# Kernel tuning notes

Hardware: AMD Instinct MI355X
Metric: run time of the kernel (lower is better)

Reference implementation:

```python
import jax, jax.numpy as jnp
import numpy as np
import math

D_MODEL = 1024
H = 16
D_K = D_MODEL // H
D_FF = 4096
NEG = -1e9


def layer_norm(x, alpha, bias):
    # Faithful to source: mean over last dim, UNBIASED std (torch.std default),
    # eps defined in source but never used in forward.
    mean = jnp.mean(x, axis=-1, keepdims=True)
    std = jnp.std(x, axis=-1, ddof=1, keepdims=True)
    return (x - mean) / std * alpha + bias


def mha(x, mask, w_q, w_k, w_v, w_o):
    B, S, D = x.shape
    q = (x @ w_q.T).reshape(B, S, H, D_K)
    k = (x @ w_k.T).reshape(B, S, H, D_K)
    v = (x @ w_v.T).reshape(B, S, H, D_K)
    scores = jnp.einsum('bqhd,bkhd->bhqk', q, k) / math.sqrt(D_K)
    scores = jnp.where(mask, NEG, scores)
    attn = jax.nn.softmax(scores, axis=-1)
    out = jnp.einsum('bhqk,bkhd->bqhd', attn, v).reshape(B, S, D)
    return out @ w_o.T


def setup_inputs() -> dict:
    key = jax.random.key(0)
    ks = jax.random.split(key, 16)
    B, S = 4, 2048
    s = 0.02
    return {
        'x': jax.random.normal(ks[0], (B, S, D_MODEL), jnp.float32),
        'w_q': jax.random.normal(ks[1], (D_MODEL, D_MODEL), jnp.float32) * s,
        'w_k': jax.random.normal(ks[2], (D_MODEL, D_MODEL), jnp.float32) * s,
        'w_v': jax.random.normal(ks[3], (D_MODEL, D_MODEL), jnp.float32) * s,
        'w_o': jax.random.normal(ks[4], (D_MODEL, D_MODEL), jnp.float32) * s,
        'l1_w': jax.random.normal(ks[5], (D_FF, D_MODEL), jnp.float32) * s,
        'l1_b': jnp.zeros((D_FF,), jnp.float32),
        'l2_w': jax.random.normal(ks[6], (D_MODEL, D_FF), jnp.float32) * s,
        'l2_b': jnp.zeros((D_MODEL,), jnp.float32),
        'norm1_a': jnp.ones((D_MODEL,), jnp.float32),
        'norm1_b': jnp.zeros((D_MODEL,), jnp.float32),
        'norm2_a': jnp.ones((D_MODEL,), jnp.float32),
        'norm2_b': jnp.zeros((D_MODEL,), jnp.float32),
        'normf_a': jnp.ones((D_MODEL,), jnp.float32),
        'normf_b': jnp.zeros((D_MODEL,), jnp.float32),
        'mask': jax.random.randint(ks[7], (B, 1, 1, S), 0, 2) == 1,
    }


def reference(x, w_q, w_k, w_v, w_o, l1_w, l1_b, l2_w, l2_b,
              norm1_a, norm1_b, norm2_a, norm2_b, normf_a, normf_b, mask):
    # residual 1: pre-norm self-attention (dropout is identity at eval)
    x = x + mha(layer_norm(x, norm1_a, norm1_b), mask, w_q, w_k, w_v, w_o)
    # residual 2: pre-norm FFN
    h = layer_norm(x, norm2_a, norm2_b)
    ff = jax.nn.relu(h @ l1_w.T + l1_b) @ l2_w.T + l2_b
    x = x + ff
    return layer_norm(x, normf_a, normf_b)
```

## Files before the change

kernel.cpp:

```cpp
#include <hip/hip_runtime.h>
#include <hip/hip_bf16.h>


typedef __bf16 bf16x8 __attribute__((ext_vector_type(8)));
typedef float f32x4 __attribute__((ext_vector_type(4)));
typedef unsigned short u16x8 __attribute__((ext_vector_type(8)));
using bf16 = __hip_bfloat16;

__device__ __forceinline__ f32x4 mfma16(bf16x8 a, bf16x8 b, f32x4 c) {
  return __builtin_amdgcn_mfma_f32_16x16x32_bf16(a, b, c, 0, 0, 0);
}

__device__ __forceinline__ int swz(int row, int blk) {
  return row * 64 + ((blk ^ (row & 7)) << 3);
}

__device__ __forceinline__ void stage_tile64(unsigned short* lds,
                                             const bf16* g, int ld, int rows) {
  const int lane = threadIdx.x & 63, wid = threadIdx.x >> 6;
  const int r8 = lane >> 3, blk = lane & 7;
  const bf16* gl = g + (size_t)r8 * ld + ((blk ^ r8) << 3);
  const int passes = rows >> 3;
  for (int p = wid; p < passes; p += 4) {
    __builtin_amdgcn_global_load_lds(
        (const __attribute__((address_space(1))) void*)(gl + (size_t)(p * 8) * ld),
        (__attribute__((address_space(3))) void*)(lds + p * 512),
        16, 0, 0);
  }
}

__device__ __forceinline__ void stage_half512(unsigned short* lds,
                                              const bf16* g, int ld) {
  const int lane = threadIdx.x & 63, w8 = threadIdx.x >> 6;
  const int r8 = lane >> 3, blk = lane & 7;
  const bf16* gl = g + (size_t)r8 * ld + ((blk ^ r8) << 3);
  __builtin_amdgcn_global_load_lds(
      (const __attribute__((address_space(1))) void*)(gl + (size_t)(w8 * 8) * ld),
      (__attribute__((address_space(3))) void*)(lds + w8 * 512), 16, 0, 0);
  __builtin_amdgcn_global_load_lds(
      (const __attribute__((address_space(1))) void*)(gl + (size_t)((w8 + 8) * 8) * ld),
      (__attribute__((address_space(3))) void*)(lds + (w8 + 8) * 512), 16, 0, 0);
}

__device__ __forceinline__ short bfb(float x) {
  return (short)__hip_bfloat16_raw(__float2bfloat16(x)).x;
}

__global__ __launch_bounds__(256) void cvt_all_k(
    const float* __restrict__ wq, const float* __restrict__ wk,
    const float* __restrict__ wv, const float* __restrict__ wo,
    const float* __restrict__ l1, const float* __restrict__ l2,
    bf16* __restrict__ WQKV, bf16* __restrict__ WO, bf16* __restrict__ L1W,
    bf16* __restrict__ L2W) {
  const int bid = blockIdx.x;
  const float* s;
  bf16* d;
  int lb;
  if (bid < 1024) {
    s = wq; d = WQKV; lb = bid;
  } else if (bid < 2048) {
    s = wk; d = WQKV + (1 << 20); lb = bid - 1024;
  } else if (bid < 3072) {
    s = wv; d = WQKV + (2 << 20); lb = bid - 2048;
  } else if (bid < 4096) {
    s = wo; d = WO; lb = bid - 3072;
  } else if (bid < 8192) {
    s = l1; d = L1W; lb = bid - 4096;
  } else {
    s = l2; d = L2W; lb = bid - 8192;
  }
  const int i = lb * 1024 + threadIdx.x * 4;
  const float4 v = *reinterpret_cast<const float4*>(s + i);
  ushort4 o;
  o.x = (unsigned short)bfb(v.x);
  o.y = (unsigned short)bfb(v.y);
  o.z = (unsigned short)bfb(v.z);
  o.w = (unsigned short)bfb(v.w);
  *reinterpret_cast<ushort4*>(d + i) = o;
}

template <bool OUT_F32>
__global__ __launch_bounds__(256) void layernorm_k(const float* __restrict__ in,
                                                   const float* __restrict__ gamma,
                                                   const float* __restrict__ beta,
                                                   void* __restrict__ out) {
  __shared__ float red[8];
  const int row = blockIdx.x, t = threadIdx.x;
  const float4 vv = reinterpret_cast<const float4*>(in + (size_t)row * 1024)[t];
  const float x0 = vv.x, x1 = vv.y, x2 = vv.z, x3 = vv.w;
  float s = x0 + x1 + x2 + x3;
#pragma unroll
  for (int off = 32; off; off >>= 1) s += __shfl_down(s, off);
  if ((t & 63) == 0) red[t >> 6] = s;
  __syncthreads();
  const float mean = (red[0] + red[1] + red[2] + red[3]) * (1.0f / 1024.0f);
  const float d0 = x0 - mean, d1 = x1 - mean, d2 = x2 - mean, d3 = x3 - mean;
  float sq = d0 * d0 + d1 * d1 + d2 * d2 + d3 * d3;
#pragma unroll
  for (int off = 32; off; off >>= 1) sq += __shfl_down(sq, off);
  if ((t & 63) == 0) red[4 + (t >> 6)] = sq;
  __syncthreads();
  const float var =
      fmaxf((red[4] + red[5] + red[6] + red[7]) * (1.0f / 1023.0f), 1e-20f);
  const float rstd = rsqrtf(var);
  const float4 ga = reinterpret_cast<const float4*>(gamma)[t];
  const float4 be = reinterpret_cast<const float4*>(beta)[t];
  const float y0 = d0 * rstd * ga.x + be.x;
  const float y1 = d1 * rstd * ga.y + be.y;
  const float y2 = d2 * rstd * ga.z + be.z;
  const float y3 = d3 * rstd * ga.w + be.w;
  if (OUT_F32) {
    reinterpret_cast<float4*>((float*)out + (size_t)row * 1024)[t] =
        make_float4(y0, y1, y2, y3);
  } else {
    ushort4 o;
    o.x = (unsigned short)bfb(y0);
    o.y = (unsigned short)bfb(y1);
    o.z = (unsigned short)bfb(y2);
    o.w = (unsigned short)bfb(y3);
    reinterpret_cast<ushort4*>((bf16*)out + (size_t)row * 1024)[t] = o;
  }
}

template <bool HAS_BIAS, bool RELU, bool HAS_RES, bool OUT_F32>
__global__ __launch_bounds__(256) void gemm_bt(const bf16* __restrict__ A,
                                               const bf16* __restrict__ W,
                                               const float* __restrict__ bias,
                                               const float* __restrict__ resid,
                                               void* __restrict__ out,
                                               int M, int N, int K,
                                               int lda, int ldw) {
  __shared__ __align__(16) unsigned short As[128 * 64];
  __shared__ __align__(16) unsigned short Bs[128 * 64];
  const int lane = threadIdx.x & 63, wid = threadIdx.x >> 6;
  const int n16 = lane & 15, quad = lane >> 4;
  const int wm = (wid >> 1) * 64, wn = (wid & 1) * 64;
  const int tm = blockIdx.x * 128, tn = blockIdx.y * 128;
  f32x4 acc[4][4] = {};
  for (int k0 = 0; k0 < K; k0 += 64) {
    stage_tile64(As, A + (size_t)tm * lda + k0, lda, 128);
    stage_tile64(Bs, W + (size_t)tn * ldw + k0, ldw, 128);
    __syncthreads();
#pragma unroll
    for (int kk = 0; kk < 64; kk += 32) {
      bf16x8 af[4], bw[4];
#pragma unroll
      for (int i = 0; i < 4; ++i)
        af[i] = *reinterpret_cast<const bf16x8*>(
            &As[swz(wm + i * 16 + n16, (kk >> 3) + quad)]);
#pragma unroll
      for (int j = 0; j < 4; ++j)
        bw[j] = *reinterpret_cast<const bf16x8*>(
            &Bs[swz(wn + j * 16 + n16, (kk >> 3) + quad)]);
#pragma unroll
      for (int i = 0; i < 4; ++i)
#pragma unroll
        for (int j = 0; j < 4; ++j) acc[i][j] = mfma16(af[i], bw[j], acc[i][j]);
    }
    __syncthreads();
  }
#pragma unroll
  for (int i = 0; i < 4; ++i) {
#pragma unroll
    for (int j = 0; j < 4; ++j) {
      const int n = tn + wn + j * 16 + n16;
      const float bv = HAS_BIAS ? bias[n] : 0.0f;
#pragma unroll
      for (int r = 0; r < 4; ++r) {
        const int m = tm + wm + i * 16 + quad * 4 + r;
        float vv = acc[i][j][r] + bv;
        if (RELU) vv = fmaxf(vv, 0.0f);
        if (HAS_RES) vv += resid[(size_t)m * N + n];
        if (OUT_F32)
          ((float*)out)[(size_t)m * N + n] = vv;
        else
          ((bf16*)out)[(size_t)m * N + n] = __float2bfloat16(vv);
      }
    }
  }
}

#define PHASE3(LAB, LBB, QB, DO_B, STAGES, WAITS)                              \
  {                                                                            \
    const unsigned short* LA = (LAB) + lasel * 8192;                           \
    if (DO_B) {                                                                \
      const unsigned short* LB = (LBB) + lbsel * 8192;                         \
      _Pragma("unroll") for (int j = 0; j < 4; ++j) {                          \
        const int br = bloc + j * 16 + n16;                                    \
        bfr[j][0] = *reinterpret_cast<const bf16x8*>(&LB[swz(br, quad)]);      \
        bfr[j][1] = *reinterpret_cast<const bf16x8*>(&LB[swz(br, 4 + quad)]);  \
      }                                                                        \
    }                                                                          \
    bf16x8 a0[4], a1[4];                                                       \
    _Pragma("unroll") for (int ii = 0; ii < 4; ++ii) {                         \
      const int ar = ((QB)*2 + ii) * 16 + n16;                                 \
      a0[ii] = *reinterpret_cast<const bf16x8*>(&LA[swz(ar, quad)]);           \
      a1[ii] = *reinterpret_cast<const bf16x8*>(&LA[swz(ar, 4 + quad)]);       \
    }                                                                          \
    STAGES;                                                                    \
    WAITS;                                                                     \
    __builtin_amdgcn_sched_barrier(0);                                         \
    __builtin_amdgcn_s_barrier();                                              \
    asm volatile("s_waitcnt lgkmcnt(0)" ::: "memory");                         \
    __builtin_amdgcn_sched_barrier(0);                                         \
    __builtin_amdgcn_s_setprio(1);                                             \
    _Pragma("unroll") for (int ii = 0; ii < 4; ++ii)                           \
        _Pragma("unroll") for (int j = 0; j < 4; ++j) {                        \
      f32x4 c = acc[(QB)*2 + ii][j];                                           \
      c = mfma16(a0[ii], bfr[j][0], c);                                        \
      c = mfma16(a1[ii], bfr[j][1], c);                                        \
      acc[(QB)*2 + ii][j] = c;                                                 \
    }                                                                          \
    __builtin_amdgcn_s_setprio(0);                                             \
    __builtin_amdgcn_sched_barrier(0);                                         \
    __builtin_amdgcn_s_barrier();                                              \
  }

template <bool QKV, bool HAS_BIAS, bool RELU>
__global__ __launch_bounds__(512, 1) void gemm256_k(
    const bf16* __restrict__ A0p, const bf16* __restrict__ cln,
    const bf16* __restrict__ W, const float* __restrict__ bias,
    const int* __restrict__ cnt, bf16* __restrict__ out,
    bf16* __restrict__ kvout, int M, int N, int K, int lda, int ldw) {
  __shared__ __align__(16) unsigned short Lds[81920];
  const int tm = blockIdx.x * 256;
  const int tn = blockIdx.y * 256;
  const bf16* A = A0p;
  bool isQ = true;
  if (QKV) {
    isQ = (blockIdx.y < 4);
    if (!isQ) {
      const int npad = (cnt[tm >> 11] + 127) & ~127;
      if ((tm & 2047) >= npad) return;
      A = cln;
    }
  }
  const int lane = threadIdx.x & 63, w8 = threadIdx.x >> 6;
  const int n16 = lane & 15, quad = lane >> 4;
  const int wm = (w8 >> 2) << 7;
  const int wn = (w8 & 3) << 6;
  const int lasel = wm >> 7, lbsel = wn >> 7, bloc = wn & 127;
  const int NTT = K >> 6;
  const bf16* Ag = A + (size_t)tm * lda;
  const bf16* Wg = W + (size_t)tn * ldw;
  f32x4 acc[8][4] = {};

  auto STAGEA = [&](int slot, int tile) {
    unsigned short* dst = Lds + slot * 16384;
    stage_half512(dst, Ag + tile * 64, lda);
    stage_half512(dst + 8192, Ag + (size_t)128 * lda + tile * 64, lda);
  };
  auto STAGEB = [&](int slot, int tile) {
    unsigned short* dst = Lds + 49152 + slot * 16384;
    stage_half512(dst, Wg + tile * 64, ldw);
    stage_half512(dst + 8192, Wg + (size_t)128 * ldw + tile * 64, ldw);
  };

  STAGEA(0, 0); STAGEB(0, 0);
  STAGEA(1, 1); STAGEB(1, 1);
  asm volatile("s_waitcnt vmcnt(8)" ::: "memory");
  __builtin_amdgcn_sched_barrier(0);
  __builtin_amdgcn_s_barrier();

  int sA = 0;
  for (int i = 0; i < NTT; i += 2) {
    const bool hasNext = (i + 2 < NTT);
    const int sA1 = (sA + 1 == 3) ? 0 : sA + 1;
    const int sA2 = (sA1 + 1 == 3) ? 0 : sA1 + 1;
    const unsigned short* LAi = Lds + sA * 16384;
    const unsigned short* LAi1 = Lds + sA1 * 16384;
    const unsigned short* LB0 = Lds + 49152;
    const unsigned short* LB1 = Lds + 49152 + 16384;
    bf16x8 bfr[4][2];
    PHASE3(LAi, LB0, 0, true, if (hasNext) STAGEA(sA2, i + 2), );
    PHASE3(LAi, LB0, 2, false, if (hasNext) STAGEB(0, i + 2),
           if (hasNext) { asm volatile("s_waitcnt vmcnt(8)" ::: "memory"); }
           else { asm volatile("s_waitcnt vmcnt(0)" ::: "memory"); });
    PHASE3(LAi1, LB1, 0, true, if (hasNext) STAGEA(sA, i + 3), );
    PHASE3(LAi1, LB1, 2, false, if (hasNext) STAGEB(1, i + 3),
           if (hasNext) { asm volatile("s_waitcnt vmcnt(8)" ::: "memory"); });
    sA = sA2;
  }
  bf16* op;
  int ldo, nc0;
  if (QKV && !isQ) {
    op = kvout; ldo = 2048; nc0 = tn - 1024;
  } else if (QKV) {
    op = out; ldo = 1024; nc0 = tn;
  } else {
    op = out; ldo = N; nc0 = tn;
  }
#pragma unroll
  for (int i = 0; i < 8; ++i) {
#pragma unroll
    for (int j = 0; j < 4; ++j) {
      const int n = nc0 + wn + j * 16 + n16;
      const float bv = HAS_BIAS ? bias[n] : 0.0f;
#pragma unroll
      for (int r = 0; r < 4; ++r) {
        const int m = tm + wm + i * 16 + quad * 4 + r;
        float vv = acc[i][j][r] + bv;
        if (RELU) vv = fmaxf(vv, 0.0f);
        op[(size_t)m * ldo + n] = __float2bfloat16(vv);
      }
    }
  }
}

__global__ __launch_bounds__(256) void prep_mask_k(const int* __restrict__ m,
                                                   float* __restrict__ mf,
                                                   int n) {
  __shared__ int s;
  if (threadIdx.x == 0) s = 0;
  __syncthreads();
  unsigned int acc = 0;
  for (int i = threadIdx.x; i < 512; i += 256)
    acc |= ((const unsigned int*)m)[i] & 0xFFFFFF00u;
  if (acc) atomicOr(&s, 1);
  __syncthreads();
  const bool bytes = (s != 0);
  const int i = blockIdx.x * 256 + threadIdx.x;
  if (i < n) {
    const int v = bytes ? (int)((const unsigned char*)m)[i] : m[i];
    mf[i] = v ? -1.4427e9f : 0.0f;
  }
}

__global__ __launch_bounds__(256) void scan_k(const float* __restrict__ maskf,
                                              float* __restrict__ cmask,
                                              int* __restrict__ idx,
                                              int* __restrict__ cnt) {
  __shared__ int wsum[4];
  const int b = blockIdx.x, t = threadIdx.x, lane = t & 63, w = t >> 6;
  const float* mrow = maskf + b * 2048;
  int keep[8], local = 0;
#pragma unroll
  for (int e = 0; e < 8; ++e) {
    keep[e] = (mrow[t * 8 + e] == 0.0f) ? 1 : 0;
    local += keep[e];
  }
  int inc = local;
#pragma unroll
  for (int off = 1; off < 64; off <<= 1) {
    int v = __shfl_up(inc, off);
    if (lane >= off) inc += v;
  }
  if (lane == 63) wsum[w] = inc;
  __syncthreads();
  int base = 0;
#pragma unroll
  for (int i = 0; i < 4; ++i)
    if (i < w) base += wsum[i];
  int p = base + inc - local;
#pragma unroll
  for (int e = 0; e < 8; ++e)
    if (keep[e]) idx[b * 2048 + p++] = t * 8 + e;
  const int total = wsum[0] + wsum[1] + wsum[2] + wsum[3];
  if (t == 0) cnt[b] = total;
  for (int i = t; i < 2048; i += 256)
    cmask[b * 2048 + i] = (i < total) ? 0.0f : -1.4427e9f;
}

__global__ __launch_bounds__(128) void gatherA_k(const bf16* __restrict__ ln1,
                                                 const int* __restrict__ idx,
                                                 const int* __restrict__ cnt,
                                                 bf16* __restrict__ cln) {
  const int b = blockIdx.x >> 11, j = blockIdx.x & 2047;
  const int n = cnt[b];
  const int npad = (n + 127) & ~127;
  if (j >= npad) return;
  u16x8* dst = reinterpret_cast<u16x8*>(cln + ((size_t)(b * 2048 + j)) * 1024);
  if (j < n) {
    const int s = idx[b * 2048 + j];
    const u16x8* src =
        reinterpret_cast<const u16x8*>(ln1 + ((size_t)(b * 2048 + s)) * 1024);
    dst[threadIdx.x] = src[threadIdx.x];
  } else {
    u16x8 z = {};
    dst[threadIdx.x] = z;
  }
}

__global__ __launch_bounds__(256) void attn_k(const bf16* __restrict__ q,
                                              const bf16* __restrict__ kv,
                                              const float* __restrict__ cmask,
                                              const int* __restrict__ cnt,
                                              bf16* __restrict__ out, int BHN) {
  __shared__ __align__(16) unsigned short Ks[2][64 * 64];
  __shared__ __align__(16) unsigned short Vs[2][64 * 72];
  const int lane = threadIdx.x & 63, wid = threadIdx.x >> 6;
  const int n16 = lane & 15, quad = lane >> 4;
  const int bid0 = blockIdx.x;
  const int nwg = gridDim.x;
  const int bid = (bid0 & 7) * (nwg >> 3) + (bid0 >> 3);
  const int qb = bid & 15, bh = bid >> 4;
  const int b = bh >> 4, h = bh & 15;
  const bf16* qp0 = q + (size_t)b * 2048 * 1024 + h * 64;
  const bf16* kp0 = kv + (size_t)b * 2048 * 2048 + h * 64;
  const bf16* vp0 = kp0 + 1024;
  const float* mfb = cmask + b * 2048;
  const int cntb = cnt[b];
  const int nk = ((cntb + 63) >> 6) << 6;
  const int qrow0 = qb * 128 + wid * 32;

  bf16x8 qf[2][2];
#pragma unroll
  for (int g = 0; g < 2; ++g) {
    const bf16* qp = qp0 + (size_t)(qrow0 + g * 16 + n16) * 1024 + quad * 8;
    qf[g][0] = *reinterpret_cast<const bf16x8*>(qp);
    qf[g][1] = *reinterpret_cast<const bf16x8*>(qp + 32);
  }
  bf16x8 ones;
#pragma unroll
  for (int e = 0; e < 8; ++e) ones[e] = (__bf16)1.0f;
  f32x4 oacc[2][4] = {};
  f32x4 lacc[2] = {};
  const int prow = ((n16 >> 2) << 3) + (n16 & 3);
  const int vkey = lane, vdc = wid * 16;

  stage_tile64(Ks[0], kp0, 2048, 64);
  {
    const bf16* vp = vp0 + (size_t)vkey * 2048 + vdc;
    const u16x8 a = *reinterpret_cast<const u16x8*>(vp);
    const u16x8 bq = *reinterpret_cast<const u16x8*>(vp + 8);
#pragma unroll
    for (int e = 0; e < 8; ++e) {
      Vs[0][(vdc + e) * 72 + vkey] = a[e];
      Vs[0][(vdc + 8 + e) * 72 + vkey] = bq[e];
    }
  }
  int cur = 0;
  for (int kt = 0; kt < nk; kt += 64) {
    __syncthreads();
    const bool hasNext = (kt + 64 < nk);
    const bool fullTile = (kt + 64 <= cntb);
    u16x8 na = {}, nb = {};
    if (hasNext) {
      stage_tile64(Ks[cur ^ 1], kp0 + (size_t)(kt + 64) * 2048, 2048, 64);
      const bf16* vp = vp0 + (size_t)(kt + 64 + vkey) * 2048 + vdc;
      na = *reinterpret_cast<const u16x8*>(vp);
      nb = *reinterpret_cast<const u16x8*>(vp + 8);
    }
    const unsigned short* Kc = Ks[cur];
    const unsigned short* Vc = Vs[cur];
#pragma unroll
    for (int sub = 0; sub < 2; ++sub) {
      const int kb = sub * 32;
      bf16x8 aflo[2], afhi[2];
#pragma unroll
      for (int st = 0; st < 2; ++st) {
        const int row = kb + prow + st * 4;
        aflo[st] = *reinterpret_cast<const bf16x8*>(&Kc[swz(row, quad)]);
        afhi[st] = *reinterpret_cast<const bf16x8*>(&Kc[swz(row, 4 + quad)]);
      }
      __builtin_amdgcn_s_setprio(1);
      f32x4 z[2][2];
#pragma unroll
      for (int g = 0; g < 2; ++g)
#pragma unroll
        for (int st = 0; st < 2; ++st) {
          f32x4 zz = {};
          zz = mfma16(aflo[st], qf[g][0], zz);
          zz = mfma16(afhi[st], qf[g][1], zz);
          z[g][st] = zz;
        }
      __builtin_amdgcn_s_setprio(0);
      float4 m0 = make_float4(0.f, 0.f, 0.f, 0.f);
      float4 m1 = make_float4(0.f, 0.f, 0.f, 0.f);
      if (!fullTile) {
        m0 = *reinterpret_cast<const float4*>(mfb + kt + kb + quad * 8);
        m1 = *reinterpret_cast<const float4*>(mfb + kt + kb + quad * 8 + 4);
      }
      bf16x8 vf[4];
#pragma unroll
      for (int j = 0; j < 4; ++j)
        vf[j] = *reinterpret_cast<const bf16x8*>(
            &Vc[(j * 16 + n16) * 72 + kb + quad * 8]);
#pragma unroll
      for (int g = 0; g < 2; ++g) {
        bf16x8 pf;
#pragma unroll
        for (int r = 0; r < 4; ++r) {
          const float e0 = __builtin_amdgcn_exp2f(
              fmaf(z[g][0][r], 0.18033688f, ((const float*)&m0)[r]));
          const float e1 = __builtin_amdgcn_exp2f(
              fmaf(z[g][1][r], 0.18033688f, ((const float*)&m1)[r]));
          pf[r] = (__bf16)e0;
          pf[4 + r] = (__bf16)e1;
        }
        __builtin_amdgcn_s_setprio(1);
#pragma unroll
        for (int j = 0; j < 4; ++j) oacc[g][j] = mfma16(pf, vf[j], oacc[g][j]);
        lacc[g] = mfma16(pf, ones, lacc[g]);
        __builtin_amdgcn_s_setprio(0);
      }
    }
    if (hasNext) {
      unsigned short* Vn = Vs[cur ^ 1];
#pragma unroll
      for (int e = 0; e < 8; ++e) {
        Vn[(vdc + e) * 72 + vkey] = na[e];
        Vn[(vdc + 8 + e) * 72 + vkey] = nb[e];
      }
    }
    cur ^= 1;
  }
#pragma unroll
  for (int g = 0; g < 2; ++g) {
#pragma unroll
    for (int r = 0; r < 4; ++r) {
      const float lr = 1.0f / fmaxf(lacc[g][r], 1e-20f);
      bf16* op =
          out + (size_t)(b * 2048 + qrow0 + g * 16 + quad * 4 + r) * 1024 +
          h * 64;
#pragma unroll
      for (int j = 0; j < 4; ++j)
        op[j * 16 + n16] = __float2bfloat16(oacc[g][j][r] * lr);
    }
  }
}

extern "C" void kernel_launch(void* const* d_in, const int* in_sizes, int n_in,
                              void* d_out, int out_size, void* d_ws,
                              size_t ws_size, hipStream_t stream) {
  const float* x    = (const float*)d_in[0];
  const float* w_q  = (const float*)d_in[1];
  const float* w_k  = (const float*)d_in[2];
  const float* w_v  = (const float*)d_in[3];
  const float* w_o  = (const float*)d_in[4];
  const float* l1_w = (const float*)d_in[5];
  const float* l1_b = (const float*)d_in[6];
  const float* l2_w = (const float*)d_in[7];
  const float* l2_b = (const float*)d_in[8];
  const float* n1a  = (const float*)d_in[9];
  const float* n1b  = (const float*)d_in[10];
  const float* n2a  = (const float*)d_in[11];
  const float* n2b  = (const float*)d_in[12];
  const float* nfa  = (const float*)d_in[13];
  const float* nfb  = (const float*)d_in[14];
  const int* mask   = (const int*)d_in[15];

  const int D = 1024, FF = 4096;
  const int M = in_sizes[0] / D;
  const int B = M / 2048;

  const size_t MB = 1024ull * 1024ull;
  if (ws_size < 121 * MB) return;
  char* w = (char*)d_ws;
  bf16* WQKV = (bf16*)(w + 0 * MB);
  bf16* WO   = (bf16*)(w + 6 * MB);
  bf16* L1W  = (bf16*)(w + 8 * MB);
  bf16* L2W  = (bf16*)(w + 16 * MB);
  bf16* LN1  = (bf16*)(w + 24 * MB);
  bf16* Qbuf = (bf16*)(w + 40 * MB);
  bf16* ATT  = LN1;
  bf16* HLN  = (bf16*)(w + 40 * MB);
  bf16* CLN  = (bf16*)(w + 56 * MB);
  bf16* FF1  = (bf16*)(w + 56 * MB);
  bf16* KV   = (bf16*)(w + 88 * MB);
  float* X1  = (float*)(w + 88 * MB);
  float* MASKF = (float*)(w + 120 * MB);
  float* CMASK = (float*)(w + 120 * MB + 256 * 1024);
  int*   IDX   = (int*)(w + 120 * MB + 512 * 1024);
  int*   CNT   = (int*)(w + 120 * MB + 768 * 1024);

  const dim3 blk(256);
  cvt_all_k<<<dim3(12288), blk, 0, stream>>>(w_q, w_k, w_v, w_o, l1_w, l2_w,
                                             WQKV, WO, L1W, L2W);
  prep_mask_k<<<dim3((M + 255) / 256), blk, 0, stream>>>(mask, MASKF, M);
  scan_k<<<dim3(B), blk, 0, stream>>>(MASKF, CMASK, IDX, CNT);

  layernorm_k<false><<<M, blk, 0, stream>>>(x, n1a, n1b, LN1);
  gatherA_k<<<dim3(B * 2048), dim3(128), 0, stream>>>(LN1, IDX, CNT, CLN);
  gemm256_k<true, false, false><<<dim3(M / 256, 12), dim3(512), 0, stream>>>(
      LN1, CLN, WQKV, nullptr, CNT, Qbuf, KV, M, 3072, 1024, 1024, 1024);
  const int BHN = B * 16;
  attn_k<<<dim3((M / 128) * 16), blk, 0, stream>>>(Qbuf, KV, CMASK, CNT, ATT,
                                                   BHN);
  gemm_bt<false, false, true, true><<<dim3(M / 128, D / 128), blk, 0, stream>>>(
      ATT, WO, nullptr, x, X1, M, D, D, D, D);
  layernorm_k<false><<<M, blk, 0, stream>>>(X1, n2a, n2b, HLN);
  for (int c = 0; c < 2; ++c) {
    gemm256_k<false, true, true><<<dim3(M / 256, 8), dim3(512), 0, stream>>>(
        HLN, nullptr, L1W + (size_t)c * 2048 * D, l1_b + c * 2048, nullptr,
        FF1, nullptr, M, 2048, 1024, 1024, 1024);
    if (c == 0)
      gemm_bt<true, false, true, true>
          <<<dim3(M / 128, D / 128), blk, 0, stream>>>(
              FF1, L2W + c * 2048, l2_b, X1, X1, M, D, 2048, 2048, FF);
    else
      gemm_bt<false, false, true, true>
          <<<dim3(M / 128, D / 128), blk, 0, stream>>>(
              FF1, L2W + c * 2048, nullptr, X1, X1, M, D, 2048, 2048, FF);
  }
  layernorm_k<true><<<M, blk, 0, stream>>>(X1, nfa, nfb, (float*)d_out);
}
```

Measured before the change: 493.4 us.

## Fuse mask prep into scan, scatter LN1 rows directly, and unsplit FFN GEMMs

Mask prep and the prefix scan now run as one kernel that emits per-row ranks and zero-pads the compacted buffer. The first layernorm scatters kept rows into it, which removes the separate gather kernel. The FFN runs as a single full-width up-projection whose output is spread across eight 512-column chunks in free workspace, followed by one down-projection GEMM. The earlier two-chunk loop with its extra residual read-modify-write pass is gone, and the l2 weight conversion moves later so its buffer can reuse space. It also folds the softmax scale into the Q projection and skips mask loads on full attention tiles. The cost is a more intricate workspace aliasing scheme and indirect chunked A addressing.

```diff
diff --git a/kernel.cpp b/kernel.cpp
--- a/kernel.cpp
+++ b/kernel.cpp
@@ -6,6 +6,8 @@
 typedef float f32x4 __attribute__((ext_vector_type(4)));
 typedef unsigned short u16x8 __attribute__((ext_vector_type(8)));
 using bf16 = __hip_bfloat16;
+
+struct Tab8 { bf16* p[8]; };
 
 __device__ __forceinline__ f32x4 mfma16(bf16x8 a, bf16x8 b, f32x4 c) {
   return __builtin_amdgcn_mfma_f32_16x16x32_bf16(a, b, c, 0, 0, 0);
@@ -46,12 +48,25 @@
   return (short)__hip_bfloat16_raw(__float2bfloat16(x)).x;
 }
 
-__global__ __launch_bounds__(256) void cvt_all_k(
+__global__ __launch_bounds__(256) void cvt_k(const float* __restrict__ s,
+                                             bf16* __restrict__ d, int n) {
+  const int i = (blockIdx.x * 256 + threadIdx.x) * 4;
+  if (i + 3 < n) {
+    const float4 v = *reinterpret_cast<const float4*>(s + i);
+    ushort4 o;
+    o.x = (unsigned short)bfb(v.x);
+    o.y = (unsigned short)bfb(v.y);
+    o.z = (unsigned short)bfb(v.z);
+    o.w = (unsigned short)bfb(v.w);
+    *reinterpret_cast<ushort4*>(d + i) = o;
+  }
+}
+
+__global__ __launch_bounds__(256) void cvt_main_k(
     const float* __restrict__ wq, const float* __restrict__ wk,
     const float* __restrict__ wv, const float* __restrict__ wo,
-    const float* __restrict__ l1, const float* __restrict__ l2,
-    bf16* __restrict__ WQKV, bf16* __restrict__ WO, bf16* __restrict__ L1W,
-    bf16* __restrict__ L2W) {
+    const float* __restrict__ l1, bf16* __restrict__ WQKV,
+    bf16* __restrict__ WO, bf16* __restrict__ L1W) {
   const int bid = blockIdx.x;
   const float* s;
   bf16* d;
@@ -64,10 +79,8 @@
     s = wv; d = WQKV + (2 << 20); lb = bid - 2048;
   } else if (bid < 4096) {
     s = wo; d = WO; lb = bid - 3072;
-  } else if (bid < 8192) {
+  } else {
     s = l1; d = L1W; lb = bid - 4096;
-  } else {
-    s = l2; d = L2W; lb = bid - 8192;
   }
   const int i = lb * 1024 + threadIdx.x * 4;
   const float4 v = *reinterpret_cast<const float4*>(s + i);
@@ -79,11 +92,69 @@
   *reinterpret_cast<ushort4*>(d + i) = o;
 }
 
-template <bool OUT_F32>
+__global__ __launch_bounds__(256) void scan2_k(const int* __restrict__ m,
+                                               float* __restrict__ cmask,
+                                               int* __restrict__ rank,
+                                               int* __restrict__ cnt,
+                                               bf16* __restrict__ cln) {
+  __shared__ int wsum[4];
+  __shared__ int sflag;
+  const int b = blockIdx.x, t = threadIdx.x, lane = t & 63, w = t >> 6;
+  if (t == 0) sflag = 0;
+  __syncthreads();
+  unsigned int acc = 0;
+  for (int i = t; i < 512; i += 256)
+    acc |= ((const unsigned int*)m)[i] & 0xFFFFFF00u;
+  if (acc) atomicOr(&sflag, 1);
+  __syncthreads();
+  const bool bytes = (sflag != 0);
+  int keep[8], local = 0;
+#pragma unroll
+  for (int e = 0; e < 8; ++e) {
+    const int g = b * 2048 + t * 8 + e;
+    const int v = bytes ? (int)((const unsigned char*)m)[g] : m[g];
+    keep[e] = (v == 0) ? 1 : 0;
+    local += keep[e];
+  }
+  int inc = local;
+#pragma unroll
+  for (int off = 1; off < 64; off <<= 1) {
+    int vv = __shfl_up(inc, off);
+    if (lane >= off) inc += vv;
+  }
+  if (lane == 63) wsum[w] = inc;
+  __syncthreads();
+  int base = 0;
+#pragma unroll
+  for (int i = 0; i < 4; ++i)
+    if (i < w) base += wsum[i];
+  int p = base + inc - local;
+#pragma unroll
+  for (int e = 0; e < 8; ++e) {
+    const int g = b * 2048 + t * 8 + e;
+    rank[g] = keep[e] ? p++ : -1;
+  }
+  const int total = wsum[0] + wsum[1] + wsum[2] + wsum[3];
+  if (t == 0) cnt[b] = total;
+  for (int i = t; i < 2048; i += 256)
+    cmask[b * 2048 + i] = (i < total) ? 0.0f : -1.4427e9f;
+  const int npad = (total + 127) & ~127;
+  const int nzero = (npad - total) * 256;
+  for (int i = t; i < nzero; i += 256) {
+    const int row = total + (i >> 8), c4 = (i & 255) * 4;
+    ushort4 z = {0, 0, 0, 0};
+    *reinterpret_cast<ushort4*>(cln + ((size_t)(b * 2048 + row)) * 1024 + c4) =
+        z;
+  }
+}
+
+template <bool OUT_F32, bool WCLN>
 __global__ __launch_bounds__(256) void layernorm_k(const float* __restrict__ in,
                                                    const float* __restrict__ gamma,
                                                    const float* __restrict__ beta,
-                                                   void* __restrict__ out) {
+                                                   void* __restrict__ out,
+                                                   const int* __restrict__ rank,
+                                                   bf16* __restrict__ cln) {
   __shared__ float red[8];
   const int row = blockIdx.x, t = threadIdx.x;
   const float4 vv = reinterpret_cast<const float4*>(in + (size_t)row * 1024)[t];
@@ -119,17 +190,23 @@
     o.z = (unsigned short)bfb(y2);
     o.w = (unsigned short)bfb(y3);
     reinterpret_cast<ushort4*>((bf16*)out + (size_t)row * 1024)[t] = o;
-  }
-}
-
-template <bool HAS_BIAS, bool RELU, bool HAS_RES, bool OUT_F32>
+    if (WCLN) {
+      const int j = rank[row];
+      if (j >= 0)
+        reinterpret_cast<ushort4*>(
+            cln + ((size_t)((row >> 11) * 2048 + j)) * 1024)[t] = o;
+    }
+  }
+}
+
+template <bool HAS_BIAS, bool RELU, bool HAS_RES, bool OUT_F32, bool CHUNKA>
 __global__ __launch_bounds__(256) void gemm_bt(const bf16* __restrict__ A,
                                                const bf16* __restrict__ W,
                                                const float* __restrict__ bias,
                                                const float* __restrict__ resid,
                                                void* __restrict__ out,
                                                int M, int N, int K,
-                                               int lda, int ldw) {
+                                               int lda, int ldw, Tab8 tabA) {
   __shared__ __align__(16) unsigned short As[128 * 64];
   __shared__ __align__(16) unsigned short Bs[128 * 64];
   const int lane = threadIdx.x & 63, wid = threadIdx.x >> 6;
@@ -138,7 +215,12 @@
   const int tm = blockIdx.x * 128, tn = blockIdx.y * 128;
   f32x4 acc[4][4] = {};
   for (int k0 = 0; k0 < K; k0 += 64) {
-    stage_tile64(As, A + (size_t)tm * lda + k0, lda, 128);
+    if (CHUNKA) {
+      const bf16* Ab = tabA.p[k0 >> 9] + (size_t)tm * 512 + (k0 & 511);
+      stage_tile64(As, Ab, 512, 128);
+    } else {
+      stage_tile64(As, A + (size_t)tm * lda + k0, lda, 128);
+    }
     stage_tile64(Bs, W + (size_t)tn * ldw + k0, ldw, 128);
     __syncthreads();
 #pragma unroll
@@ -216,18 +298,19 @@
     __builtin_amdgcn_s_barrier();                                              \
   }
 
-template <bool QKV, bool HAS_BIAS, bool RELU>
+template <int MODE>
 __global__ __launch_bounds__(512, 1) void gemm256_k(
     const bf16* __restrict__ A0p, const bf16* __restrict__ cln,
     const bf16* __restrict__ W, const float* __restrict__ bias,
     const int* __restrict__ cnt, bf16* __restrict__ out,
-    bf16* __restrict__ kvout, int M, int N, int K, int lda, int ldw) {
+    bf16* __restrict__ kvout, Tab8 tabO, int M, int N, int K, int lda,
+    int ldw) {
   __shared__ __align__(16) unsigned short Lds[81920];
   const int tm = blockIdx.x * 256;
   const int tn = blockIdx.y * 256;
   const bf16* A = A0p;
   bool isQ = true;
-  if (QKV) {
+  if (MODE == 0) {
     isQ = (blockIdx.y < 4);
     if (!isQ) {
       const int npad = (cnt[tm >> 11] + 127) & ~127;
@@ -281,103 +364,45 @@
            if (hasNext) { asm volatile("s_waitcnt vmcnt(8)" ::: "memory"); });
     sA = sA2;
   }
-  bf16* op;
-  int ldo, nc0;
-  if (QKV && !isQ) {
-    op = kvout; ldo = 2048; nc0 = tn - 1024;
-  } else if (QKV) {
-    op = out; ldo = 1024; nc0 = tn;
+  if (MODE == 1) {
+    bf16* op = tabO.p[tn >> 9];
+    const int col0 = tn & 511;
+#pragma unroll
+    for (int i = 0; i < 8; ++i) {
+#pragma unroll
+      for (int j = 0; j < 4; ++j) {
+        const int nn = wn + j * 16 + n16;
+        const float bv = bias[tn + nn];
+#pragma unroll
+        for (int r = 0; r < 4; ++r) {
+          const int m = tm + wm + i * 16 + quad * 4 + r;
+          float vv = fmaxf(acc[i][j][r] + bv, 0.0f);
+          op[(size_t)m * 512 + col0 + nn] = __float2bfloat16(vv);
+        }
+      }
+    }
   } else {
-    op = out; ldo = N; nc0 = tn;
-  }
-#pragma unroll
-  for (int i = 0; i < 8; ++i) {
-#pragma unroll
-    for (int j = 0; j < 4; ++j) {
-      const int n = nc0 + wn + j * 16 + n16;
-      const float bv = HAS_BIAS ? bias[n] : 0.0f;
-#pragma unroll
-      for (int r = 0; r < 4; ++r) {
-        const int m = tm + wm + i * 16 + quad * 4 + r;
-        float vv = acc[i][j][r] + bv;
-        if (RELU) vv = fmaxf(vv, 0.0f);
-        op[(size_t)m * ldo + n] = __float2bfloat16(vv);
+    bf16* op;
+    int ldo, nc0;
+    float scale = 1.0f;
+    if (!isQ) {
+      op = kvout; ldo = 2048; nc0 = tn - 1024;
+    } else {
+      op = out; ldo = 1024; nc0 = tn;
+      scale = 0.18033688f;
+    }
+#pragma unroll
+    for (int i = 0; i < 8; ++i) {
+#pragma unroll
+      for (int j = 0; j < 4; ++j) {
+        const int n = nc0 + wn + j * 16 + n16;
+#pragma unroll
+        for (int r = 0; r < 4; ++r) {
+          const int m = tm + wm + i * 16 + quad * 4 + r;
+          op[(size_t)m * ldo + n] = __float2bfloat16(acc[i][j][r] * scale);
+        }
       }
     }
-  }
-}
-
-__global__ __launch_bounds__(256) void prep_mask_k(const int* __restrict__ m,
-                                                   float* __restrict__ mf,
-                                                   int n) {
-  __shared__ int s;
-  if (threadIdx.x == 0) s = 0;
-  __syncthreads();
-  unsigned int acc = 0;
-  for (int i = threadIdx.x; i < 512; i += 256)
-    acc |= ((const unsigned int*)m)[i] & 0xFFFFFF00u;
-  if (acc) atomicOr(&s, 1);
-  __syncthreads();
-  const bool bytes = (s != 0);
-  const int i = blockIdx.x * 256 + threadIdx.x;
-  if (i < n) {
-    const int v = bytes ? (int)((const unsigned char*)m)[i] : m[i];
-    mf[i] = v ? -1.4427e9f : 0.0f;
-  }
-}
-
-__global__ __launch_bounds__(256) void scan_k(const float* __restrict__ maskf,
-                                              float* __restrict__ cmask,
-                                              int* __restrict__ idx,
-                                              int* __restrict__ cnt) {
-  __shared__ int wsum[4];
-  const int b = blockIdx.x, t = threadIdx.x, lane = t & 63, w = t >> 6;
-  const float* mrow = maskf + b * 2048;
-  int keep[8], local = 0;
-#pragma unroll
-  for (int e = 0; e < 8; ++e) {
-    keep[e] = (mrow[t * 8 + e] == 0.0f) ? 1 : 0;
-    local += keep[e];
-  }
-  int inc = local;
-#pragma unroll
-  for (int off = 1; off < 64; off <<= 1) {
-    int v = __shfl_up(inc, off);
-    if (lane >= off) inc += v;
-  }
-  if (lane == 63) wsum[w] = inc;
-  __syncthreads();
-  int base = 0;
-#pragma unroll
-  for (int i = 0; i < 4; ++i)
-    if (i < w) base += wsum[i];
-  int p = base + inc - local;
-#pragma unroll
-  for (int e = 0; e < 8; ++e)
-    if (keep[e]) idx[b * 2048 + p++] = t * 8 + e;
-  const int total = wsum[0] + wsum[1] + wsum[2] + wsum[3];
-  if (t == 0) cnt[b] = total;
-  for (int i = t; i < 2048; i += 256)
-    cmask[b * 2048 + i] = (i < total) ? 0.0f : -1.4427e9f;
-}
-
-__global__ __launch_bounds__(128) void gatherA_k(const bf16* __restrict__ ln1,
-                                                 const int* __restrict__ idx,
-                                                 const int* __restrict__ cnt,
-                                                 bf16* __restrict__ cln) {
-  const int b = blockIdx.x >> 11, j = blockIdx.x & 2047;
-  const int n = cnt[b];
-  const int npad = (n + 127) & ~127;
-  if (j >= npad) return;
-  u16x8* dst = reinterpret_cast<u16x8*>(cln + ((size_t)(b * 2048 + j)) * 1024);
-  if (j < n) {
-    const int s = idx[b * 2048 + j];
-    const u16x8* src =
-        reinterpret_cast<const u16x8*>(ln1 + ((size_t)(b * 2048 + s)) * 1024);
-    dst[threadIdx.x] = src[threadIdx.x];
-  } else {
-    u16x8 z = {};
-    dst[threadIdx.x] = z;
   }
 }
 
@@ -465,34 +490,49 @@
           z[g][st] = zz;
         }
       __builtin_amdgcn_s_setprio(0);
-      float4 m0 = make_float4(0.f, 0.f, 0.f, 0.f);
-      float4 m1 = make_float4(0.f, 0.f, 0.f, 0.f);
-      if (!fullTile) {
-        m0 = *reinterpret_cast<const float4*>(mfb + kt + kb + quad * 8);
-        m1 = *reinterpret_cast<const float4*>(mfb + kt + kb + quad * 8 + 4);
-      }
       bf16x8 vf[4];
 #pragma unroll
       for (int j = 0; j < 4; ++j)
         vf[j] = *reinterpret_cast<const bf16x8*>(
             &Vc[(j * 16 + n16) * 72 + kb + quad * 8]);
-#pragma unroll
-      for (int g = 0; g < 2; ++g) {
-        bf16x8 pf;
-#pragma unroll
-        for (int r = 0; r < 4; ++r) {
-          const float e0 = __builtin_amdgcn_exp2f(
-              fmaf(z[g][0][r], 0.18033688f, ((const float*)&m0)[r]));
-          const float e1 = __builtin_amdgcn_exp2f(
-              fmaf(z[g][1][r], 0.18033688f, ((const float*)&m1)[r]));
-          pf[r] = (__bf16)e0;
-          pf[4 + r] = (__bf16)e1;
+      if (fullTile) {
+#pragma unroll
+        for (int g = 0; g < 2; ++g) {
+          bf16x8 pf;
+#pragma unroll
+          for (int r = 0; r < 4; ++r) {
+            pf[r] = (__bf16)__builtin_amdgcn_exp2f(z[g][0][r]);
+            pf[4 + r] = (__bf16)__builtin_amdgcn_exp2f(z[g][1][r]);
+          }
+          __builtin_amdgcn_s_setprio(1);
+#pragma unroll
+          for (int j = 0; j < 4; ++j)
+            oacc[g][j] = mfma16(pf, vf[j], oacc[g][j]);
+          lacc[g] = mfma16(pf, ones, lacc[g]);
+          __builtin_amdgcn_s_setprio(0);
         }
-        __builtin_amdgcn_s_setprio(1);
-#pragma unroll
-        for (int j = 0; j < 4; ++j) oacc[g][j] = mfma16(pf, vf[j], oacc[g][j]);
-        lacc[g] = mfma16(pf, ones, lacc[g]);
-        __builtin_amdgcn_s_setprio(0);
+      } else {
+        const float4 m0 =
+            *reinterpret_cast<const float4*>(mfb + kt + kb + quad * 8);
+        const float4 m1 =
+            *reinterpret_cast<const float4*>(mfb + kt + kb + quad * 8 + 4);
+#pragma unroll
+        for (int g = 0; g < 2; ++g) {
+          bf16x8 pf;
+#pragma unroll
+          for (int r = 0; r < 4; ++r) {
+            pf[r] = (__bf16)__builtin_amdgcn_exp2f(z[g][0][r] +
+                                                   ((const float*)&m0)[r]);
+            pf[4 + r] = (__bf16)__builtin_amdgcn_exp2f(z[g][1][r] +
+                                                       ((const float*)&m1)[r]);
+          }
+          __builtin_amdgcn_s_setprio(1);
+#pragma unroll
+          for (int j = 0; j < 4; ++j)
+            oacc[g][j] = mfma16(pf, vf[j], oacc[g][j]);
+          lacc[g] = mfma16(pf, ones, lacc[g]);
+          __builtin_amdgcn_s_setprio(0);
+        }
       }
     }
     if (hasNext) {
@@ -550,48 +590,52 @@
   bf16* WQKV = (bf16*)(w + 0 * MB);
   bf16* WO   = (bf16*)(w + 6 * MB);
   bf16* L1W  = (bf16*)(w + 8 * MB);
-  bf16* L2W  = (bf16*)(w + 16 * MB);
   bf16* LN1  = (bf16*)(w + 24 * MB);
   bf16* Qbuf = (bf16*)(w + 40 * MB);
   bf16* ATT  = LN1;
   bf16* HLN  = (bf16*)(w + 40 * MB);
+  bf16* L2W  = (bf16*)(w + 40 * MB);
   bf16* CLN  = (bf16*)(w + 56 * MB);
-  bf16* FF1  = (bf16*)(w + 56 * MB);
   bf16* KV   = (bf16*)(w + 88 * MB);
   float* X1  = (float*)(w + 88 * MB);
-  float* MASKF = (float*)(w + 120 * MB);
-  float* CMASK = (float*)(w + 120 * MB + 256 * 1024);
-  int*   IDX   = (int*)(w + 120 * MB + 512 * 1024);
-  int*   CNT   = (int*)(w + 120 * MB + 768 * 1024);
+  float* CMASK = (float*)(w + 120 * MB);
+  int*   RANK  = (int*)(w + 120 * MB + 64 * 1024);
+  int*   CNT   = (int*)(w + 120 * MB + 192 * 1024);
+
+  Tab8 ff1;
+  ff1.p[0] = (bf16*)(w + 0 * MB);
+  ff1.p[1] = (bf16*)(w + 16 * MB);
+  ff1.p[2] = (bf16*)(w + 24 * MB);
+  ff1.p[3] = (bf16*)(w + 32 * MB);
+  ff1.p[4] = (bf16*)(w + 56 * MB);
+  ff1.p[5] = (bf16*)(w + 64 * MB);
+  ff1.p[6] = (bf16*)(w + 72 * MB);
+  ff1.p[7] = (bf16*)(w + 80 * MB);
+  Tab8 dummy = {};
 
   const dim3 blk(256);
-  cvt_all_k<<<dim3(12288), blk, 0, stream>>>(w_q, w_k, w_v, w_o, l1_w, l2_w,
-                                             WQKV, WO, L1W, L2W);
-  prep_mask_k<<<dim3((M + 255) / 256), blk, 0, stream>>>(mask, MASKF, M);
-  scan_k<<<dim3(B), blk, 0, stream>>>(MASKF, CMASK, IDX, CNT);
-
-  layernorm_k<false><<<M, blk, 0, stream>>>(x, n1a, n1b, LN1);
-  gatherA_k<<<dim3(B * 2048), dim3(128), 0, stream>>>(LN1, IDX, CNT, CLN);
-  gemm256_k<true, false, false><<<dim3(M / 256, 12), dim3(512), 0, stream>>>(
-      LN1, CLN, WQKV, nullptr, CNT, Qbuf, KV, M, 3072, 1024, 1024, 1024);
+  cvt_main_k<<<dim3(8192), blk, 0, stream>>>(w_q, w_k, w_v, w_o, l1_w, WQKV,
+                                             WO, L1W);
+  scan2_k<<<dim3(B), blk, 0, stream>>>(mask, CMASK, RANK, CNT, CLN);
+  layernorm_k<false, true><<<M, blk, 0, stream>>>(x, n1a, n1b, LN1, RANK, CLN);
+  gemm256_k<0><<<dim3(M / 256, 12), dim3(512), 0, stream>>>(
+      LN1, CLN, WQKV, nullptr, CNT, Qbuf, KV, dummy, M, 3072, 1024, 1024,
+      1024);
   const int BHN = B * 16;
   attn_k<<<dim3((M / 128) * 16), blk, 0, stream>>>(Qbuf, KV, CMASK, CNT, ATT,
                                                    BHN);
-  gemm_bt<false, false, true, true><<<dim3(M / 128, D / 128), blk, 0, stream>>>(
-      ATT, WO, nullptr, x, X1, M, D, D, D, D);
-  layernorm_k<false><<<M, blk, 0, stream>>>(X1, n2a, n2b, HLN);
-  for (int c = 0; c < 2; ++c) {
-    gemm256_k<false, true, true><<<dim3(M / 256, 8), dim3(512), 0, stream>>>(
-        HLN, nullptr, L1W + (size_t)c * 2048 * D, l1_b + c * 2048, nullptr,
-        FF1, nullptr, M, 2048, 1024, 1024, 1024);
-    if (c == 0)
-      gemm_bt<true, false, true, true>
-          <<<dim3(M / 128, D / 128), blk, 0, stream>>>(
-              FF1, L2W + c * 2048, l2_b, X1, X1, M, D, 2048, 2048, FF);
-    else
-      gemm_bt<false, false, true, true>
-          <<<dim3(M / 128, D / 128), blk, 0, stream>>>(
-              FF1, L2W + c * 2048, nullptr, X1, X1, M, D, 2048, 2048, FF);
-  }
-  layernorm_k<true><<<M, blk, 0, stream>>>(X1, nfa, nfb, (float*)d_out);
-}
+  gemm_bt<false, false, true, true, false>
+      <<<dim3(M / 128, D / 128), blk, 0, stream>>>(ATT, WO, nullptr, x, X1, M,
+                                                   D, D, D, D, dummy);
+  layernorm_k<false, false><<<M, blk, 0, stream>>>(X1, n2a, n2b, HLN, nullptr,
+                                                   nullptr);
+  gemm256_k<1><<<dim3(M / 256, 16), dim3(512), 0, stream>>>(
+      HLN, nullptr, L1W, l1_b, nullptr, nullptr, nullptr, ff1, M, FF, 1024,
+      1024, 1024);
+  cvt_k<<<dim3(FF * D / 1024), blk, 0, stream>>>(l2_w, L2W, FF * D);
+  gemm_bt<true, false, true, true, true>
+      <<<dim3(M / 128, D / 128), blk, 0, stream>>>(nullptr, L2W, l2_b, X1, X1,
+                                                   M, D, FF, 512, FF, ff1);
+  layernorm_k<true, false><<<M, blk, 0, stream>>>(X1, nfa, nfb, (float*)d_out,
+                                                  nullptr, nullptr);
+}
```

New measurement: 479.9 us. 1.03x faster.
